# Kernel optimization log

Measured on AMD Instinct MI355X. Metric: run time of the kernel, lower is better.

Reference implementation:

```python
import jax, jax.numpy as jnp
import numpy as np

H = 8  # num_heads

def setup_inputs() -> dict:
    key = jax.random.key(0)
    k1, k2, k3, k4 = jax.random.split(key, 4)
    B, T, D, K = 16, 8192, 512, 4
    x = jax.random.normal(k1, (B, T, D), dtype=jnp.float32)
    mask = jax.random.randint(k2, (B, T), 0, 2, dtype=jnp.int32)
    queries = jax.random.normal(k3, (1, K, D), dtype=jnp.float32) * 0.02
    # xavier_uniform for (D, D) Linear weight
    limit = np.sqrt(6.0 / (D + D))
    w_out = jax.random.uniform(k4, (D, D), dtype=jnp.float32, minval=-limit, maxval=limit)
    b_out = jnp.zeros((D,), dtype=jnp.float32)
    return {"x": x, "mask": mask, "queries": queries, "w_out": w_out, "b_out": b_out}

def reference(x, mask, queries, w_out, b_out):
    B, T, D = x.shape
    K = queries.shape[1]
    hd = D // H
    scale = jnp.sqrt(jnp.float32(hd))
    q = queries.reshape(K, H, hd)          # shared across batch
    kv = x.reshape(B, T, H, hd)            # keys == values
    scores = jnp.einsum('khd,bthd->bhkt', q, kv) / scale  # (B,H,K,T)
    scores = jnp.where(mask[:, None, None, :] == 0, jnp.float32(-1e9), scores)
    attn = jax.nn.softmax(scores, axis=-1)  # dropout is identity in eval / p=0
    out = jnp.einsum('bhkt,bthd->bkhd', attn, kv).reshape(B, K, D)
    return out @ w_out.T + b_out
```

## Files before the change

### kernel.cpp

```cpp
#include <hip/hip_runtime.h>
#include <math.h>

#define BB 16
#define TT 8192
#define DD 512
#define KK 4
#define HH 8
#define HD 64

__global__ __launch_bounds__(256, 2)
void attn_partial_kernel(const float* __restrict__ x,
                         const int* __restrict__ mask,
                         const float* __restrict__ queries,
                         float* __restrict__ ws,
                         int NC) {
    const int C     = TT / NC;
    const int iters = C >> 3;
    const int b     = blockIdx.x / NC;
    const int c     = blockIdx.x % NC;
    const int t0    = c * C;
    const int tid   = threadIdx.x;
    const int slot  = tid >> 5;
    const int seg   = tid & 31;
    const int h     = seg >> 2;
    const int qd    = seg & 3;

    __shared__ int    smask[512];
    __shared__ float4 smerge[8 * 512];
    __shared__ float  smerge_l[8 * 32];

    for (int i = tid; i < C; i += 256) smask[i] = mask[b * TT + t0 + i];
    __syncthreads();

    const float4* q4 = reinterpret_cast<const float4*>(queries);
    float4 qv[4][4];
    #pragma unroll
    for (int k = 0; k < 4; ++k)
        #pragma unroll
        for (int j = 0; j < 4; ++j) {
            float4 v = q4[k * 128 + seg * 4 + j];
            v.x *= 0.125f; v.y *= 0.125f; v.z *= 0.125f; v.w *= 0.125f;
            qv[k][j] = v;
        }

    float4 av[4][4];
    #pragma unroll
    for (int k = 0; k < 4; ++k)
        #pragma unroll
        for (int j = 0; j < 4; ++j) av[k][j] = make_float4(0.f, 0.f, 0.f, 0.f);
    float l[4] = {0.f, 0.f, 0.f, 0.f};

    const float4* xp = reinterpret_cast<const float4*>(x) +
                       ((size_t)(b * TT + t0 + slot)) * 128 + seg * 4;

    float4 pf[4];
    #pragma unroll
    for (int j = 0; j < 4; ++j) pf[j] = xp[j];
    int mv = smask[slot];

    for (int i = 0; i < iters; ++i) {
        float4 xc[4];
        #pragma unroll
        for (int j = 0; j < 4; ++j) xc[j] = pf[j];
        const int mc = mv;
        if (i + 1 < iters) {
            xp += 1024;
            #pragma unroll
            for (int j = 0; j < 4; ++j) pf[j] = xp[j];
            mv = smask[8 * (i + 1) + slot];
        }

        float s[4];
        #pragma unroll
        for (int k = 0; k < 4; ++k) {
            float a = 0.f;
            #pragma unroll
            for (int j = 0; j < 4; ++j) {
                a = fmaf(qv[k][j].x, xc[j].x, a);
                a = fmaf(qv[k][j].y, xc[j].y, a);
                a = fmaf(qv[k][j].z, xc[j].z, a);
                a = fmaf(qv[k][j].w, xc[j].w, a);
            }
            s[k] = a;
        }
        #pragma unroll
        for (int k = 0; k < 4; ++k) {
            s[k] += __shfl_xor(s[k], 1);
            s[k] += __shfl_xor(s[k], 2);
        }

        float w[4];
        #pragma unroll
        for (int k = 0; k < 4; ++k) w[k] = mc ? __expf(s[k]) : 0.f;
        #pragma unroll
        for (int k = 0; k < 4; ++k) {
            l[k] += w[k];
            #pragma unroll
            for (int j = 0; j < 4; ++j) {
                av[k][j].x = fmaf(w[k], xc[j].x, av[k][j].x);
                av[k][j].y = fmaf(w[k], xc[j].y, av[k][j].y);
                av[k][j].z = fmaf(w[k], xc[j].z, av[k][j].z);
                av[k][j].w = fmaf(w[k], xc[j].w, av[k][j].w);
            }
        }
    }

    #pragma unroll
    for (int k = 0; k < 4; ++k)
        #pragma unroll
        for (int j = 0; j < 4; ++j)
            smerge[slot * 512 + (h * 4 + k) * 16 + qd * 4 + j] = av[k][j];
    if (qd == 0) {
        #pragma unroll
        for (int k = 0; k < 4; ++k) smerge_l[slot * 32 + h * 4 + k] = l[k];
    }
    __syncthreads();

    float4* O4 = reinterpret_cast<float4*>(ws);
    const size_t obase = ((size_t)b * NC + c) * 512;
    for (int f = tid; f < 512; f += 256) {
        float4 sacc = smerge[f];
        #pragma unroll
        for (int s2 = 1; s2 < 8; ++s2) {
            float4 v = smerge[s2 * 512 + f];
            sacc.x += v.x; sacc.y += v.y; sacc.z += v.z; sacc.w += v.w;
        }
        O4[obase + f] = sacc;
    }
    if (tid < 32) {
        float sacc = 0.f;
        #pragma unroll
        for (int s2 = 0; s2 < 8; ++s2) sacc += smerge_l[s2 * 32 + tid];
        float* lp = ws + (size_t)BB * NC * HH * KK * 64;
        lp[(((size_t)b * NC + c) * HH + (tid >> 2)) * KK + (tid & 3)] = sacc;
    }
}

__global__ __launch_bounds__(256, 4)
void merge_gemm_kernel(const float* __restrict__ ws,
                       const float* __restrict__ w_out,
                       const float* __restrict__ b_out,
                       float* __restrict__ out,
                       int NC) {
    const int bk  = blockIdx.x;
    const int b   = bk >> 2;
    const int k   = bk & 3;
    const int tid = threadIdx.x;

    __shared__ __align__(16) float row[512];
    __shared__ float linv[8];

    if (tid < 8) {
        const float* lp = ws + (size_t)BB * NC * HH * KK * 64;
        float s = 0.f;
        for (int c = 0; c < NC; ++c)
            s += lp[(((size_t)b * NC + c) * HH + tid) * KK + k];
        linv[tid] = 1.0f / s;
    }
    __syncthreads();

    for (int item = tid; item < 512; item += 256) {
        const int h = item >> 6, d = item & 63;
        float s = 0.f;
        for (int c = 0; c < NC; ++c)
            s += ws[((((size_t)b * NC + c) * HH + h) * KK + k) * 64 + d];
        row[item] = s * linv[h];
    }
    __syncthreads();

    const float4* W4 = reinterpret_cast<const float4*>(w_out);
    const float4* R4 = reinterpret_cast<const float4*>(row);
    float a0 = b_out[tid];
    float a1 = b_out[tid + 256];
    for (int d4 = 0; d4 < 128; ++d4) {
        const float4 r  = R4[d4];
        const float4 wa = W4[(size_t)tid * 128 + d4];
        const float4 wb = W4[((size_t)tid + 256) * 128 + d4];
        a0 = fmaf(r.x, wa.x, fmaf(r.y, wa.y, fmaf(r.z, wa.z, fmaf(r.w, wa.w, a0))));
        a1 = fmaf(r.x, wb.x, fmaf(r.y, wb.y, fmaf(r.z, wb.z, fmaf(r.w, wb.w, a1))));
    }
    out[(size_t)bk * 512 + tid]       = a0;
    out[(size_t)bk * 512 + tid + 256] = a1;
}

extern "C" void kernel_launch(void* const* d_in, const int* in_sizes, int n_in,
                              void* d_out, int out_size, void* d_ws, size_t ws_size,
                              hipStream_t stream) {
    const float* x       = (const float*)d_in[0];
    const int*   mask    = (const int*)d_in[1];
    const float* queries = (const float*)d_in[2];
    const float* w_out   = (const float*)d_in[3];
    const float* b_out   = (const float*)d_in[4];
    float*       out     = (float*)d_out;
    float*       ws      = (float*)d_ws;

    int NC = 32;
    while (NC > 16 && (size_t)BB * NC * HH * KK * 65 * 4 > ws_size) NC >>= 1;

    attn_partial_kernel<<<BB * NC, 256, 0, stream>>>(x, mask, queries, ws, NC);
    merge_gemm_kernel<<<BB * KK, 256, 0, stream>>>(ws, w_out, b_out, out, NC);
}
```

Baseline: 417.6 us.

## Split each row across full wavefront and double-buffer prefetch with 512-thread blocks

After: 421.2 us. About the same (+0.9%).

```diff
diff --git a/kernel.cpp b/kernel.cpp
--- a/kernel.cpp
+++ b/kernel.cpp
@@ -8,7 +8,7 @@
 #define HH 8
 #define HD 64
 
-__global__ __launch_bounds__(256, 2)
+__global__ __launch_bounds__(512, 4)
 void attn_partial_kernel(const float* __restrict__ x,
                          const int* __restrict__ mask,
                          const float* __restrict__ queries,
@@ -20,87 +20,128 @@
     const int c     = blockIdx.x % NC;
     const int t0    = c * C;
     const int tid   = threadIdx.x;
-    const int slot  = tid >> 5;
-    const int seg   = tid & 31;
-    const int h     = seg >> 2;
-    const int qd    = seg & 3;
+    const int slot  = tid >> 6;
+    const int seg   = tid & 63;
+    const int h     = seg >> 3;
+    const int qd    = seg & 7;
 
     __shared__ int    smask[512];
     __shared__ float4 smerge[8 * 512];
     __shared__ float  smerge_l[8 * 32];
 
-    for (int i = tid; i < C; i += 256) smask[i] = mask[b * TT + t0 + i];
+    for (int i = tid; i < C; i += 512) smask[i] = mask[b * TT + t0 + i];
     __syncthreads();
 
     const float4* q4 = reinterpret_cast<const float4*>(queries);
-    float4 qv[4][4];
+    float4 qv[4][2];
     #pragma unroll
     for (int k = 0; k < 4; ++k)
         #pragma unroll
-        for (int j = 0; j < 4; ++j) {
-            float4 v = q4[k * 128 + seg * 4 + j];
+        for (int j = 0; j < 2; ++j) {
+            float4 v = q4[k * 128 + seg * 2 + j];
             v.x *= 0.125f; v.y *= 0.125f; v.z *= 0.125f; v.w *= 0.125f;
             qv[k][j] = v;
         }
 
-    float4 av[4][4];
+    float4 av[4][2];
     #pragma unroll
     for (int k = 0; k < 4; ++k)
         #pragma unroll
-        for (int j = 0; j < 4; ++j) av[k][j] = make_float4(0.f, 0.f, 0.f, 0.f);
+        for (int j = 0; j < 2; ++j) av[k][j] = make_float4(0.f, 0.f, 0.f, 0.f);
     float l[4] = {0.f, 0.f, 0.f, 0.f};
 
     const float4* xp = reinterpret_cast<const float4*>(x) +
-                       ((size_t)(b * TT + t0 + slot)) * 128 + seg * 4;
-
-    float4 pf[4];
-    #pragma unroll
-    for (int j = 0; j < 4; ++j) pf[j] = xp[j];
-    int mv = smask[slot];
-
-    for (int i = 0; i < iters; ++i) {
-        float4 xc[4];
-        #pragma unroll
-        for (int j = 0; j < 4; ++j) xc[j] = pf[j];
-        const int mc = mv;
-        if (i + 1 < iters) {
-            xp += 1024;
-            #pragma unroll
-            for (int j = 0; j < 4; ++j) pf[j] = xp[j];
-            mv = smask[8 * (i + 1) + slot];
-        }
-
-        float s[4];
-        #pragma unroll
-        for (int k = 0; k < 4; ++k) {
-            float a = 0.f;
-            #pragma unroll
-            for (int j = 0; j < 4; ++j) {
-                a = fmaf(qv[k][j].x, xc[j].x, a);
-                a = fmaf(qv[k][j].y, xc[j].y, a);
-                a = fmaf(qv[k][j].z, xc[j].z, a);
-                a = fmaf(qv[k][j].w, xc[j].w, a);
-            }
-            s[k] = a;
-        }
-        #pragma unroll
-        for (int k = 0; k < 4; ++k) {
-            s[k] += __shfl_xor(s[k], 1);
-            s[k] += __shfl_xor(s[k], 2);
-        }
-
-        float w[4];
-        #pragma unroll
-        for (int k = 0; k < 4; ++k) w[k] = mc ? __expf(s[k]) : 0.f;
-        #pragma unroll
-        for (int k = 0; k < 4; ++k) {
-            l[k] += w[k];
-            #pragma unroll
-            for (int j = 0; j < 4; ++j) {
-                av[k][j].x = fmaf(w[k], xc[j].x, av[k][j].x);
-                av[k][j].y = fmaf(w[k], xc[j].y, av[k][j].y);
-                av[k][j].z = fmaf(w[k], xc[j].z, av[k][j].z);
-                av[k][j].w = fmaf(w[k], xc[j].w, av[k][j].w);
+                       ((size_t)(b * TT + t0 + slot)) * 128 + seg * 2;
+
+    float4 pA0 = xp[0], pA1 = xp[1];
+    int    mA  = smask[slot];
+    float4 pB0 = xp[1024], pB1 = xp[1025];
+    int    mB  = smask[8 + slot];
+    xp += 2048;
+
+    for (int i = 0; i < iters; i += 2) {
+        {
+            const float4 x0 = pA0, x1 = pA1;
+            const int    mc = mA;
+            if (i + 2 < iters) {
+                pA0 = xp[0]; pA1 = xp[1];
+                mA  = smask[8 * (i + 2) + slot];
+                xp += 1024;
+            }
+            float s[4];
+            #pragma unroll
+            for (int k = 0; k < 4; ++k) {
+                float a;
+                a = qv[k][0].x * x0.x;
+                a = fmaf(qv[k][0].y, x0.y, a);
+                a = fmaf(qv[k][0].z, x0.z, a);
+                a = fmaf(qv[k][0].w, x0.w, a);
+                a = fmaf(qv[k][1].x, x1.x, a);
+                a = fmaf(qv[k][1].y, x1.y, a);
+                a = fmaf(qv[k][1].z, x1.z, a);
+                a = fmaf(qv[k][1].w, x1.w, a);
+                s[k] = a;
+            }
+            #pragma unroll
+            for (int k = 0; k < 4; ++k) {
+                s[k] += __shfl_xor(s[k], 1);
+                s[k] += __shfl_xor(s[k], 2);
+                s[k] += __shfl_xor(s[k], 4);
+            }
+            #pragma unroll
+            for (int k = 0; k < 4; ++k) {
+                const float w = mc ? __expf(s[k]) : 0.f;
+                l[k] += w;
+                av[k][0].x = fmaf(w, x0.x, av[k][0].x);
+                av[k][0].y = fmaf(w, x0.y, av[k][0].y);
+                av[k][0].z = fmaf(w, x0.z, av[k][0].z);
+                av[k][0].w = fmaf(w, x0.w, av[k][0].w);
+                av[k][1].x = fmaf(w, x1.x, av[k][1].x);
+                av[k][1].y = fmaf(w, x1.y, av[k][1].y);
+                av[k][1].z = fmaf(w, x1.z, av[k][1].z);
+                av[k][1].w = fmaf(w, x1.w, av[k][1].w);
+            }
+        }
+        {
+            const float4 x0 = pB0, x1 = pB1;
+            const int    mc = mB;
+            if (i + 3 < iters) {
+                pB0 = xp[0]; pB1 = xp[1];
+                mB  = smask[8 * (i + 3) + slot];
+                xp += 1024;
+            }
+            float s[4];
+            #pragma unroll
+            for (int k = 0; k < 4; ++k) {
+                float a;
+                a = qv[k][0].x * x0.x;
+                a = fmaf(qv[k][0].y, x0.y, a);
+                a = fmaf(qv[k][0].z, x0.z, a);
+                a = fmaf(qv[k][0].w, x0.w, a);
+                a = fmaf(qv[k][1].x, x1.x, a);
+                a = fmaf(qv[k][1].y, x1.y, a);
+                a = fmaf(qv[k][1].z, x1.z, a);
+                a = fmaf(qv[k][1].w, x1.w, a);
+                s[k] = a;
+            }
+            #pragma unroll
+            for (int k = 0; k < 4; ++k) {
+                s[k] += __shfl_xor(s[k], 1);
+                s[k] += __shfl_xor(s[k], 2);
+                s[k] += __shfl_xor(s[k], 4);
+            }
+            #pragma unroll
+            for (int k = 0; k < 4; ++k) {
+                const float w = mc ? __expf(s[k]) : 0.f;
+                l[k] += w;
+                av[k][0].x = fmaf(w, x0.x, av[k][0].x);
+                av[k][0].y = fmaf(w, x0.y, av[k][0].y);
+                av[k][0].z = fmaf(w, x0.z, av[k][0].z);
+                av[k][0].w = fmaf(w, x0.w, av[k][0].w);
+                av[k][1].x = fmaf(w, x1.x, av[k][1].x);
+                av[k][1].y = fmaf(w, x1.y, av[k][1].y);
+                av[k][1].z = fmaf(w, x1.z, av[k][1].z);
+                av[k][1].w = fmaf(w, x1.w, av[k][1].w);
             }
         }
     }
@@ -108,8 +149,8 @@
     #pragma unroll
     for (int k = 0; k < 4; ++k)
         #pragma unroll
-        for (int j = 0; j < 4; ++j)
-            smerge[slot * 512 + (h * 4 + k) * 16 + qd * 4 + j] = av[k][j];
+        for (int j = 0; j < 2; ++j)
+            smerge[slot * 512 + (h * 4 + k) * 16 + qd * 2 + j] = av[k][j];
     if (qd == 0) {
         #pragma unroll
         for (int k = 0; k < 4; ++k) smerge_l[slot * 32 + h * 4 + k] = l[k];
@@ -118,14 +159,14 @@
 
     float4* O4 = reinterpret_cast<float4*>(ws);
     const size_t obase = ((size_t)b * NC + c) * 512;
-    for (int f = tid; f < 512; f += 256) {
-        float4 sacc = smerge[f];
+    {
+        float4 sacc = smerge[tid];
         #pragma unroll
         for (int s2 = 1; s2 < 8; ++s2) {
-            float4 v = smerge[s2 * 512 + f];
+            float4 v = smerge[s2 * 512 + tid];
             sacc.x += v.x; sacc.y += v.y; sacc.z += v.z; sacc.w += v.w;
         }
-        O4[obase + f] = sacc;
+        O4[obase + tid] = sacc;
     }
     if (tid < 32) {
         float sacc = 0.f;
@@ -197,6 +238,6 @@
     int NC = 32;
     while (NC > 16 && (size_t)BB * NC * HH * KK * 65 * 4 > ws_size) NC >>= 1;
 
-    attn_partial_kernel<<<BB * NC, 256, 0, stream>>>(x, mask, queries, ws, NC);
+    attn_partial_kernel<<<BB * NC, 512, 0, stream>>>(x, mask, queries, ws, NC);
     merge_gemm_kernel<<<BB * KK, 256, 0, stream>>>(ws, w_out, b_out, out, NC);
 }
```
